# Kernel tuning notes

Measured on AMD Instinct MI355X. Metric: run time of the kernel, lower is better.

Reference implementation:

```python
import jax, jax.numpy as jnp
import numpy as np

ROWS, COLS, H, W = 128, 128, 128, 128
B, C = 2, 16
DENSITY = 0.01  # classic Hough vote matrix is very sparse binary


def setup_inputs() -> dict:
    key = jax.random.key(0)
    k_img, k_vote = jax.random.split(key)
    image = jax.random.normal(k_img, (B, C, ROWS, COLS), dtype=jnp.float32)
    # sparse binary voting matrix, shape (rows, cols, h, w)
    vote_index = (jax.random.uniform(k_vote, (ROWS, COLS, H, W)) < DENSITY).astype(jnp.float32)
    return {"image": image, "vote_index": vote_index}


def reference(image, vote_index):
    rows, cols, h, w = vote_index.shape
    b, c = image.shape[0], image.shape[1]
    V = vote_index.reshape(rows * cols, h * w)          # (rows*cols, h*w)
    x = jax.nn.relu(image.reshape(b * c, rows * cols))  # (b*c, rows*cols)
    ht = (x @ V) / cols                                 # (b*c, h*w)
    return ht.reshape(b, c, h, w)
```

## Files before the change

### kernel.cpp

```cpp
#include <hip/hip_runtime.h>

constexpr int Mdim = 32;
constexpr int Kdim = 16384;
constexpr int Ndim = 16384;

constexpr int TPB = 256;

constexpr int KT     = 8;
constexpr int KC     = Kdim / KT;
constexpr int SLABS  = KC / 16;
constexpr int NT32   = Ndim / 32;
constexpr int NBLK   = NT32 * KT / 4;
constexpr int DEPTH  = 4;

typedef short bf16x8 __attribute__((ext_vector_type(8)));
typedef float f32x16 __attribute__((ext_vector_type(16)));

__device__ __forceinline__ short f32_to_bf16(float f) {
    union { float f; unsigned u; } c; c.f = f;
    unsigned u = c.u;
    u += 0x7fffu + ((u >> 16) & 1u);
    return (short)(u >> 16);
}

__global__ __launch_bounds__(TPB)
void build_xa(const float* __restrict__ image, short* __restrict__ xa) {
    const int g    = blockIdx.x * TPB + threadIdx.x;
    const int lane = g & 63;
    const int slab = g >> 6;
    const int m    = lane & 31;
    const int k    = slab * 16 + (lane >> 5) * 8;
    const float* src = image + (size_t)m * Kdim + k;

    bf16x8 o;
    #pragma unroll
    for (int j = 0; j < 8; ++j)
        o[j] = f32_to_bf16(fmaxf(src[j], 0.0f) * (1.0f / 128.0f));
    reinterpret_cast<bf16x8*>(xa)[g] = o;
}

__global__ __launch_bounds__(TPB, 4)
void ht_gemm(const short* __restrict__ xa,
             const float* __restrict__ vote,
             float* __restrict__ parts)
{
    const int tid  = threadIdx.x;
    const int lane = tid & 63;
    const int w    = tid >> 6;
    const int wv   = blockIdx.x * 4 + w;
    const int nt   = wv & (NT32 - 1);
    const int kch  = wv >> 9;
    const int k0   = kch * KC;

    const int col  = nt * 32 + (lane & 31);
    const int krow = (lane >> 5) * 8;

    const float* vbase = vote + (size_t)(k0 + krow) * Ndim + col;
    const short* abase = xa + ((size_t)(k0 / 16) * 64 + lane) * 8;

    f32x16 acc;
    #pragma unroll
    for (int i = 0; i < 16; ++i) acc[i] = 0.0f;

    float  bv[DEPTH][8];
    bf16x8 av[DEPTH];

    auto load = [&](int slot, int s) {
        const float* p = vbase + (size_t)s * 16 * Ndim;
        #pragma unroll
        for (int j = 0; j < 8; ++j)
            bv[slot][j] = __builtin_nontemporal_load(p + (size_t)j * Ndim);
        av[slot] = *reinterpret_cast<const bf16x8*>(abase + (size_t)s * 512);
    };
    auto comp = [&](int slot) {
        bf16x8 f;
        #pragma unroll
        for (int j = 0; j < 8; ++j) f[j] = f32_to_bf16(bv[slot][j]);
        acc = __builtin_amdgcn_mfma_f32_32x32x16_bf16(av[slot], f, acc, 0, 0, 0);
    };

    #pragma unroll
    for (int u = 0; u < DEPTH; ++u) load(u, u);
    for (int s = 0; s < SLABS; s += DEPTH) {
        #pragma unroll
        for (int u = 0; u < DEPTH; ++u) {
            comp(u);
            if (s + DEPTH + u < SLABS) load(u, s + DEPTH + u);
        }
    }

    float* pb = parts + (size_t)kch * ((size_t)Mdim * Ndim);
    const int rbase = 4 * (lane >> 5);
    #pragma unroll
    for (int r = 0; r < 16; ++r) {
        const int row = (r & 3) + 8 * (r >> 2) + rbase;
        pb[(size_t)row * Ndim + col] = acc[r];
    }
}

__global__ __launch_bounds__(TPB)
void ht_reduce(const float* __restrict__ parts, float* __restrict__ out, int nchunks) {
    const size_t i4 = (size_t)blockIdx.x * TPB + threadIdx.x;
    const float4* p = reinterpret_cast<const float4*>(parts) + i4;
    float4 s = make_float4(0.f, 0.f, 0.f, 0.f);
    constexpr size_t stride4 = (size_t)Mdim * Ndim / 4;
    for (int c = 0; c < nchunks; ++c) {
        const float4 v = p[(size_t)c * stride4];
        s.x += v.x; s.y += v.y; s.z += v.z; s.w += v.w;
    }
    reinterpret_cast<float4*>(out)[i4] = s;
}

__global__ __launch_bounds__(TPB)
void ht_gemm_atomic(const float* __restrict__ image, const float* __restrict__ vote,
                    float* __restrict__ out) {
    __shared__ float xsh[256 * Mdim];
    const int tid = threadIdx.x;
    const int ntile = blockIdx.x % 16;
    const int k0 = (blockIdx.x / 16) * 256;
    const int nn0 = ntile * 1024 + tid * 4;
    for (int idx = tid; idx < 256 * Mdim; idx += TPB) {
        const int kk = idx >> 5, m = idx & 31;
        xsh[idx] = fmaxf(image[(size_t)m * Kdim + (k0 + kk)], 0.0f) * (1.0f / 128.0f);
    }
    __syncthreads();
    float4 acc[Mdim];
    #pragma unroll
    for (int m = 0; m < Mdim; ++m) acc[m] = make_float4(0.f, 0.f, 0.f, 0.f);
    const float* vptr = vote + (size_t)k0 * Ndim + nn0;
    for (int kk = 0; kk < 256; ++kk) {
        const float4 v = *reinterpret_cast<const float4*>(vptr);
        vptr += Ndim;
        #pragma unroll
        for (int m = 0; m < Mdim; ++m) {
            const float s = xsh[kk * Mdim + m];
            acc[m].x = fmaf(s, v.x, acc[m].x); acc[m].y = fmaf(s, v.y, acc[m].y);
            acc[m].z = fmaf(s, v.z, acc[m].z); acc[m].w = fmaf(s, v.w, acc[m].w);
        }
    }
    #pragma unroll
    for (int m = 0; m < Mdim; ++m) {
        float* o = out + (size_t)m * Ndim + nn0;
        unsafeAtomicAdd(o + 0, acc[m].x); unsafeAtomicAdd(o + 1, acc[m].y);
        unsafeAtomicAdd(o + 2, acc[m].z); unsafeAtomicAdd(o + 3, acc[m].w);
    }
}

extern "C" void kernel_launch(void* const* d_in, const int* in_sizes, int n_in,
                              void* d_out, int out_size, void* d_ws, size_t ws_size,
                              hipStream_t stream) {
    const float* image = (const float*)d_in[0];
    const float* vote  = (const float*)d_in[1];
    float* out = (float*)d_out;

    const size_t xa_bytes    = (size_t)(Kdim / 16) * 64 * 8 * sizeof(short);
    const size_t chunk_bytes = (size_t)Mdim * Ndim * sizeof(float);

    if (xa_bytes + (size_t)KT * chunk_bytes > ws_size) {
        (void)hipMemsetAsync(out, 0, (size_t)out_size * sizeof(float), stream);
        ht_gemm_atomic<<<dim3(16 * 64), TPB, 0, stream>>>(image, vote, out);
        return;
    }

    short* xa    = (short*)d_ws;
    float* parts = (float*)((char*)d_ws + xa_bytes);

    build_xa<<<dim3((Kdim / 16) * 64 / TPB), TPB, 0, stream>>>(image, xa);
    ht_gemm<<<dim3(NBLK), TPB, 0, stream>>>(xa, vote, parts);
    ht_reduce<<<dim3((Mdim * Ndim) / (4 * TPB)), TPB, 0, stream>>>(parts, out, KT);
}
```

Before: 1.298 ms.

## Widen GEMM wave tile to 64 columns with two accumulators, rolled ring buffer

Each wave now computes two adjacent 32-column MFMA tiles, so one A fragment load feeds two MFMAs and each load batch issues twice as many vote loads. This halves the number of waves and blocks. To fit the doubled registers, prefetch depth drops from 4 to 3 and the occupancy hint goes from 4 to 2. The slab loop is no longer unrolled and picks its ring-buffer slot at runtime. Indexing the register arrays dynamically like this risks the compiler moving them to scratch memory or emitting select chains.

```diff
diff --git a/kernel.cpp b/kernel.cpp
--- a/kernel.cpp
+++ b/kernel.cpp
@@ -9,9 +9,10 @@
 constexpr int KT     = 8;
 constexpr int KC     = Kdim / KT;
 constexpr int SLABS  = KC / 16;
-constexpr int NT32   = Ndim / 32;
-constexpr int NBLK   = NT32 * KT / 4;
-constexpr int DEPTH  = 4;
+constexpr int NP64   = Ndim / 64;
+constexpr int NWAVES = NP64 * KT;
+constexpr int NBLK   = NWAVES / 4;
+constexpr int DEPTH  = 3;
 
 typedef short bf16x8 __attribute__((ext_vector_type(8)));
 typedef float f32x16 __attribute__((ext_vector_type(16)));
@@ -39,7 +40,7 @@
     reinterpret_cast<bf16x8*>(xa)[g] = o;
 }
 
-__global__ __launch_bounds__(TPB, 4)
+__global__ __launch_bounds__(TPB, 2)
 void ht_gemm(const short* __restrict__ xa,
              const float* __restrict__ vote,
              float* __restrict__ parts)
@@ -48,45 +49,50 @@
     const int lane = tid & 63;
     const int w    = tid >> 6;
     const int wv   = blockIdx.x * 4 + w;
-    const int nt   = wv & (NT32 - 1);
-    const int kch  = wv >> 9;
+    const int np   = wv & (NP64 - 1);
+    const int kch  = wv >> 8;
     const int k0   = kch * KC;
 
-    const int col  = nt * 32 + (lane & 31);
+    const int col0 = np * 64 + (lane & 31);
     const int krow = (lane >> 5) * 8;
 
-    const float* vbase = vote + (size_t)(k0 + krow) * Ndim + col;
+    const float* vbase = vote + (size_t)(k0 + krow) * Ndim + col0;
     const short* abase = xa + ((size_t)(k0 / 16) * 64 + lane) * 8;
 
-    f32x16 acc;
+    f32x16 acc0, acc1;
     #pragma unroll
-    for (int i = 0; i < 16; ++i) acc[i] = 0.0f;
+    for (int i = 0; i < 16; ++i) { acc0[i] = 0.0f; acc1[i] = 0.0f; }
 
-    float  bv[DEPTH][8];
+    float  bv[DEPTH][16];
     bf16x8 av[DEPTH];
 
     auto load = [&](int slot, int s) {
         const float* p = vbase + (size_t)s * 16 * Ndim;
         #pragma unroll
-        for (int j = 0; j < 8; ++j)
-            bv[slot][j] = __builtin_nontemporal_load(p + (size_t)j * Ndim);
+        for (int j = 0; j < 8; ++j) {
+            bv[slot][j]     = __builtin_nontemporal_load(p + (size_t)j * Ndim);
+            bv[slot][8 + j] = __builtin_nontemporal_load(p + (size_t)j * Ndim + 32);
+        }
         av[slot] = *reinterpret_cast<const bf16x8*>(abase + (size_t)s * 512);
     };
     auto comp = [&](int slot) {
-        bf16x8 f;
+        bf16x8 f0, f1;
         #pragma unroll
-        for (int j = 0; j < 8; ++j) f[j] = f32_to_bf16(bv[slot][j]);
-        acc = __builtin_amdgcn_mfma_f32_32x32x16_bf16(av[slot], f, acc, 0, 0, 0);
+        for (int j = 0; j < 8; ++j) {
+            f0[j] = f32_to_bf16(bv[slot][j]);
+            f1[j] = f32_to_bf16(bv[slot][8 + j]);
+        }
+        acc0 = __builtin_amdgcn_mfma_f32_32x32x16_bf16(av[slot], f0, acc0, 0, 0, 0);
+        acc1 = __builtin_amdgcn_mfma_f32_32x32x16_bf16(av[slot], f1, acc1, 0, 0, 0);
     };
 
     #pragma unroll
     for (int u = 0; u < DEPTH; ++u) load(u, u);
-    for (int s = 0; s < SLABS; s += DEPTH) {
-        #pragma unroll
-        for (int u = 0; u < DEPTH; ++u) {
-            comp(u);
-            if (s + DEPTH + u < SLABS) load(u, s + DEPTH + u);
-        }
+    int slot = 0;
+    for (int s = 0; s < SLABS; ++s) {
+        comp(slot);
+        if (s + DEPTH < SLABS) load(slot, s + DEPTH);
+        slot = (slot + 1 == DEPTH) ? 0 : slot + 1;
     }
 
     float* pb = parts + (size_t)kch * ((size_t)Mdim * Ndim);
@@ -94,7 +100,8 @@
     #pragma unroll
     for (int r = 0; r < 16; ++r) {
         const int row = (r & 3) + 8 * (r >> 2) + rbase;
-        pb[(size_t)row * Ndim + col] = acc[r];
+        pb[(size_t)row * Ndim + col0]      = acc0[r];
+        pb[(size_t)row * Ndim + col0 + 32] = acc1[r];
     }
 }
 
```

After: 1.723 ms. 1.33x slower.
